# Kernel optimization log

Hardware: AMD Instinct MI355X
Metric: run time of the kernel (lower is better)

The kernel has to match this reference:

```python
import jax, jax.numpy as jnp
import numpy as np

N_NODES = 50000
N_EDGES = 1600000
N_GRAPHS = 512
HID = 64


def _mlp_params(key, din, dout, scale=0.1):
    k1, k2, k3 = jax.random.split(key, 3)
    return (
        jax.random.normal(k1, (din, HID), jnp.float32) * scale, jnp.zeros((HID,), jnp.float32),
        jax.random.normal(k2, (HID, HID), jnp.float32) * scale, jnp.zeros((HID,), jnp.float32),
        jax.random.normal(k3, (HID, dout), jnp.float32) * scale, jnp.zeros((dout,), jnp.float32),
    )


def _mlp(x, w1, b1, w2, b2, w3, b3, out_act=None):
    h = jax.nn.relu(x @ w1 + b1)
    h = jax.nn.relu(h @ w2 + b2)
    o = h @ w3 + b3
    return o if out_act is None else out_act(o)


def setup_inputs() -> dict:
    key = jax.random.key(0)
    ks = jax.random.split(key, 8)
    nf = jax.random.normal(ks[0], (N_NODES, 1), jnp.float32)
    ef = jax.random.normal(ks[1], (N_EDGES, 1), jnp.float32)
    src = jax.random.randint(ks[2], (N_EDGES,), 0, N_NODES)
    dst = jax.random.randint(ks[3], (N_EDGES,), 0, N_NODES)
    graph_id = jnp.sort(jax.random.randint(ks[4], (N_NODES,), 0, N_GRAPHS))
    e_w1, e_b1, e_w2, e_b2, e_w3, e_b3 = _mlp_params(ks[5], 3, 1)   # edge model: [src_nf, dst_nf, ef] -> msg
    n_w1, n_b1, n_w2, n_b2, n_w3, n_b3 = _mlp_params(ks[6], 2, 1)   # node model: [nf, agg] -> unf
    m_w1, m_b1, m_w2, m_b2, m_w3, m_b3 = _mlp_params(ks[7], 1, 1)   # node-wise MLP with Sigmoid out_act
    return dict(nf=nf, ef=ef, src=src, dst=dst, graph_id=graph_id,
                e_w1=e_w1, e_b1=e_b1, e_w2=e_w2, e_b2=e_b2, e_w3=e_w3, e_b3=e_b3,
                n_w1=n_w1, n_b1=n_b1, n_w2=n_w2, n_b2=n_b2, n_w3=n_w3, n_b3=n_b3,
                m_w1=m_w1, m_b1=m_b1, m_w2=m_w2, m_b2=m_b2, m_w3=m_w3, m_b3=m_b3)


def reference(nf, ef, src, dst, graph_id,
              e_w1, e_b1, e_w2, e_b2, e_w3, e_b3,
              n_w1, n_b1, n_w2, n_b2, n_w3, n_b3,
              m_w1, m_b1, m_w2, m_b2, m_w3, m_b3):
    # MPNN layer: message on edges, sum-aggregate to dst nodes, node update
    em_in = jnp.concatenate([nf[src], nf[dst], ef], axis=-1)          # [E, 3]
    msg = _mlp(em_in, e_w1, e_b1, e_w2, e_b2, e_w3, e_b3)             # [E, 1]
    agg = jax.ops.segment_sum(msg, dst, num_segments=N_NODES)        # [N, 1]
    unf = _mlp(jnp.concatenate([nf, agg], axis=-1),
               n_w1, n_b1, n_w2, n_b2, n_w3, n_b3)                    # [N, 1]
    # node-wise MLP with Sigmoid output activation
    node_out = _mlp(unf, m_w1, m_b1, m_w2, m_b2, m_w3, m_b3,
                    out_act=jax.nn.sigmoid)                           # [N, 1]
    # sum readout per graph, then final sigmoid
    rd = jax.ops.segment_sum(node_out, graph_id, num_segments=N_GRAPHS)  # [G, 1]
    return jax.nn.sigmoid(rd)
```

## Files before the change

### kernel.cpp

```cpp
#include <hip/hip_runtime.h>
#include <math.h>

#define HID 64
#define BKT_SHIFT 13
#define BKT_RANGE 8192
#define CCHUNK 32

typedef __attribute__((ext_vector_type(8))) short short8;
typedef __attribute__((ext_vector_type(4))) float f32x4;
typedef unsigned long long ull;

union FragU {
    uint4 q;
    short8 v;
    uint32_t u[4];
};

__device__ __forceinline__ uint32_t cvt_pk_bf16(float lo, float hi) {
    uint32_t r;
    asm("v_cvt_pk_bf16_f32 %0, %1, %2" : "=v"(r) : "v"(lo), "v"(hi));
    return r;
}
__device__ __forceinline__ float bf16lo_f(uint32_t u) { return __uint_as_float(u << 16); }
__device__ __forceinline__ float bf16hi_f(uint32_t u) { return __uint_as_float(u & 0xFFFF0000u); }
__device__ __forceinline__ unsigned short bf16_of(float v) {
    return (unsigned short)(cvt_pk_bf16(v, 0.f) & 0xFFFFu);
}

__global__ void prep_kernel(
    const float* __restrict__ w1,  const float* __restrict__ b1,  const float* __restrict__ w2,
    const float* __restrict__ nw1, const float* __restrict__ nb1, const float* __restrict__ nw2,
    const float* __restrict__ mw1, const float* __restrict__ mb1, const float* __restrict__ mw2,
    unsigned short* __restrict__ w1x,  unsigned short* __restrict__ w2T,
    unsigned short* __restrict__ nw1x, unsigned short* __restrict__ nw2T,
    unsigned short* __restrict__ mw1x, unsigned short* __restrict__ mw2T)
{
    int t = blockIdx.x * 256 + threadIdx.x;
    if (t < 4096) {
        int j = t >> 6, k = t & 63;
        w2T [t] = bf16_of(w2 [k * HID + j]);
        nw2T[t] = bf16_of(nw2[k * HID + j]);
        mw2T[t] = bf16_of(mw2[k * HID + j]);
    }
    if (t < 512) {
        int j = t >> 3, k = t & 7;
        float ve = k == 0 ? w1[j] : k == 1 ? w1[HID + j] : k == 2 ? w1[2 * HID + j] : k == 3 ? b1[j] : 0.f;
        float vn = k == 0 ? nw1[j] : k == 1 ? nw1[HID + j] : k == 2 ? nb1[j] : 0.f;
        float vm = k == 0 ? mw1[j] : k == 1 ? mb1[j] : 0.f;
        w1x [t] = bf16_of(ve);
        nw1x[t] = bf16_of(vn);
        mw1x[t] = bf16_of(vm);
    }
}

__global__ __launch_bounds__(256, 4) void edge_mfma6_kernel(
    const float* __restrict__ nf, const float* __restrict__ ef,
    const int* __restrict__ src, const int* __restrict__ dst,
    const unsigned short* __restrict__ w1x, const unsigned short* __restrict__ w2T,
    const float* __restrict__ b2, const float* __restrict__ w3, const float* __restrict__ b3,
    uint2* __restrict__ recs, ull* __restrict__ offs,
    float* __restrict__ aggFb, int E, int B, int nbatch, int mode)
{
    __shared__ uint2 tile[4][2][16][16];

    const int tid  = threadIdx.x;
    const int lane = tid & 63;
    const int wid  = tid >> 6;
    const int g    = lane >> 4;
    const int eL   = lane & 15;

    FragU af1[4];
#pragma unroll
    for (int t = 0; t < 4; ++t) {
        uint4 q = *(const uint4*)&w1x[(t * 16 + eL) * 8];
        af1[t].q = (g == 0) ? q : make_uint4(0, 0, 0, 0);
    }
    FragU af2[4][2];
#pragma unroll
    for (int t = 0; t < 4; ++t)
#pragma unroll
        for (int h = 0; h < 2; ++h)
            af2[t][h].q = *(const uint4*)&w2T[(t * 16 + eL) * 64 + h * 32 + g * 8];

    f32x4 b2v4[4];
    uint32_t w3p[8];
#pragma unroll
    for (int t = 0; t < 4; ++t) {
        int j = t * 16 + g * 4;
        b2v4[t] = *(const f32x4*)&b2[j];
        f32x4 wv = *(const f32x4*)&w3[j];
        w3p[2 * t]     = cvt_pk_bf16(wv[0], wv[1]);
        w3p[2 * t + 1] = cvt_pk_bf16(wv[2], wv[3]);
    }
    const float b3c = b3[0];

    int bi   = blockIdx.x;
    if (bi >= nbatch) return;
    int eidx = bi * 256 + tid;
    int ei   = eidx < E ? eidx : E - 1;
    int dcur = dst[ei];
    float a  = nf[src[ei]];
    float b  = nf[dcur];
    float c  = ef[ei];

    for (;;) {
        const int nbi   = bi + gridDim.x;
        const bool hn   = nbi < nbatch;
        const int neidx = hn ? nbi * 256 + tid : eidx;
        const int nei   = neidx < E ? neidx : E - 1;
        const int ns    = src[nei];
        const int nd    = dst[nei];
        const float ncf = ef[nei];

        float na = 0.f, nb = 0.f;
        float mymsg = 0.f;

#pragma unroll
        for (int ph = 0; ph < 2; ++ph) {
#pragma unroll
            for (int ss = 0; ss < 2; ++ss) {
                const int s = 2 * ph + ss;
                float av = __shfl(a, s * 16 + eL);
                float bv = __shfl(b, s * 16 + eL);
                float cv = __shfl(c, s * 16 + eL);
                FragU bin;
                bin.u[0] = (g == 0) ? cvt_pk_bf16(av, bv) : 0u;
                bin.u[1] = (g == 0) ? cvt_pk_bf16(cv, 1.0f) : 0u;
                bin.u[2] = 0u; bin.u[3] = 0u;
#pragma unroll
                for (int t = 0; t < 4; ++t) {
                    f32x4 h4 = __builtin_amdgcn_mfma_f32_16x16x32_bf16(
                        af1[t].v, bin.v, (f32x4){0.f, 0.f, 0.f, 0.f}, 0, 0, 0);
                    uint32_t p0 = cvt_pk_bf16(fmaxf(h4[0], 0.f), fmaxf(h4[1], 0.f));
                    uint32_t p1 = cvt_pk_bf16(fmaxf(h4[2], 0.f), fmaxf(h4[3], 0.f));
                    tile[wid][ss][eL][(4 * t + g) ^ ((eL & 7) << 1)] = make_uint2(p0, p1);
                }
            }

            if (ph == 0) {
                na = nf[ns];
                nb = nf[nd];
            }

#pragma unroll
            for (int ss = 0; ss < 2; ++ss) {
                const int s = 2 * ph + ss;
                const uint4* row = (const uint4*)&tile[wid][ss][eL][0];
                FragU bf0, bf1;
                bf0.q = row[(g)     ^ (eL & 7)];
                bf1.q = row[(4 + g) ^ (eL & 7)];

                float q0, q1, q2, q3;
                {
                    f32x4 ac = __builtin_amdgcn_mfma_f32_16x16x32_bf16(af2[0][0].v, bf0.v, b2v4[0], 0, 0, 0);
                    ac = __builtin_amdgcn_mfma_f32_16x16x32_bf16(af2[0][1].v, bf1.v, ac, 0, 0, 0);
                    q0 = fmaxf(ac[0], 0.f) * bf16lo_f(w3p[0]);
                    q0 = fmaf(fmaxf(ac[1], 0.f), bf16hi_f(w3p[0]), q0);
                    q0 = fmaf(fmaxf(ac[2], 0.f), bf16lo_f(w3p[1]), q0);
                    q0 = fmaf(fmaxf(ac[3], 0.f), bf16hi_f(w3p[1]), q0);
                }
                {
                    f32x4 ac = __builtin_amdgcn_mfma_f32_16x16x32_bf16(af2[1][0].v, bf0.v, b2v4[1], 0, 0, 0);
                    ac = __builtin_amdgcn_mfma_f32_16x16x32_bf16(af2[1][1].v, bf1.v, ac, 0, 0, 0);
                    q1 = fmaxf(ac[0], 0.f) * bf16lo_f(w3p[2]);
                    q1 = fmaf(fmaxf(ac[1], 0.f), bf16hi_f(w3p[2]), q1);
                    q1 = fmaf(fmaxf(ac[2], 0.f), bf16lo_f(w3p[3]), q1);
                    q1 = fmaf(fmaxf(ac[3], 0.f), bf16hi_f(w3p[3]), q1);
                }
                {
                    f32x4 ac = __builtin_amdgcn_mfma_f32_16x16x32_bf16(af2[2][0].v, bf0.v, b2v4[2], 0, 0, 0);
                    ac = __builtin_amdgcn_mfma_f32_16x16x32_bf16(af2[2][1].v, bf1.v, ac, 0, 0, 0);
                    q2 = fmaxf(ac[0], 0.f) * bf16lo_f(w3p[4]);
                    q2 = fmaf(fmaxf(ac[1], 0.f), bf16hi_f(w3p[4]), q2);
                    q2 = fmaf(fmaxf(ac[2], 0.f), bf16lo_f(w3p[5]), q2);
                    q2 = fmaf(fmaxf(ac[3], 0.f), bf16hi_f(w3p[5]), q2);
                }
                {
                    f32x4 ac = __builtin_amdgcn_mfma_f32_16x16x32_bf16(af2[3][0].v, bf0.v, b2v4[3], 0, 0, 0);
                    ac = __builtin_amdgcn_mfma_f32_16x16x32_bf16(af2[3][1].v, bf1.v, ac, 0, 0, 0);
                    q3 = fmaxf(ac[0], 0.f) * bf16lo_f(w3p[6]);
                    q3 = fmaf(fmaxf(ac[1], 0.f), bf16hi_f(w3p[6]), q3);
                    q3 = fmaf(fmaxf(ac[2], 0.f), bf16lo_f(w3p[7]), q3);
                    q3 = fmaf(fmaxf(ac[3], 0.f), bf16hi_f(w3p[7]), q3);
                }
                float p = (q0 + q1) + (q2 + q3);
                p += __shfl_xor(p, 16);
                p += __shfl_xor(p, 32);
                if (s == g) mymsg = p + b3c;
            }
        }

        const bool valid = eidx < E;

        if (mode == 1) {
            if (valid) atomicAdd(&aggFb[dcur], mymsg);
        } else {
            const int bkt = dcur >> BKT_SHIFT;
            const ull lt = (1ull << lane) - 1;
            int myslot = 0;
            int off = 0;
            uint32_t pack_lo = 0, pack_hi = 0;
            for (int bb = 0; bb < B; ++bb) {
                if (bb < 4) pack_lo |= (uint32_t)off << (8 * bb);
                else        pack_hi |= (uint32_t)off << (8 * (bb - 4));
                ull m = __ballot(valid && bkt == bb);
                if (valid && bkt == bb) myslot = off + (int)__popcll(m & lt);
                off += (int)__popcll(m);
            }
            pack_hi |= (uint32_t)off << 24;

            const size_t wgl = (size_t)bi * 4 + wid;
            if (valid) recs[wgl * 64 + myslot] = make_uint2((uint32_t)dcur, __float_as_uint(mymsg));
            if (lane == 0) offs[wgl] = ((ull)pack_hi << 32) | (ull)pack_lo;
        }

        if (!hn) break;
        bi = nbi; eidx = neidx; ei = nei;
        a = na; b = nb; c = ncf; dcur = nd;
    }
}

__global__ __launch_bounds__(256) void bucket_accum_kernel(
    const uint2* __restrict__ recs, const ull* __restrict__ offs,
    float* __restrict__ partial, int NW, int B)
{
    __shared__ float acc[BKT_RANGE];

    const int b = blockIdx.x / CCHUNK;
    const int c = blockIdx.x % CCHUNK;

    for (int i = threadIdx.x; i < BKT_RANGE; i += 256) acc[i] = 0.f;
    __syncthreads();

    const int wpc = (NW + CCHUNK - 1) / CCHUNK;
    const int w0 = c * wpc;
    const int w1 = (w0 + wpc < NW) ? w0 + wpc : NW;
    const int nb = b + 1;
    const int base_node = b << BKT_SHIFT;

    for (int w = w0 + threadIdx.x; w < w1; w += 256) {
        ull ov = offs[w];
        uint32_t lo = (uint32_t)ov, hi = (uint32_t)(ov >> 32);
        int ob = (int)(((b  < 4) ? (lo >> (8 * b))  : (hi >> (8 * (b  - 4)))) & 0xFF);
        int oe = (int)(((nb < 4) ? (lo >> (8 * nb)) : (hi >> (8 * (nb - 4)))) & 0xFF);
        const uint2* rb = recs + (size_t)w * 64;
        for (int r = ob; r < oe; ++r) {
            uint2 rec = rb[r];
            atomicAdd(&acc[(int)rec.x - base_node], __uint_as_float(rec.y));
        }
    }
    __syncthreads();

    float* pb = partial + ((size_t)b * CCHUNK + c) * BKT_RANGE;
    for (int i = threadIdx.x; i < BKT_RANGE; i += 256) pb[i] = acc[i];
}

__global__ __launch_bounds__(256) void bucket_reduce_kernel(
    const float* __restrict__ partial, float* __restrict__ agg, int N)
{
    int n = blockIdx.x * 256 + threadIdx.x;
    if (n >= N) return;
    int b = n >> BKT_SHIFT, nl = n & (BKT_RANGE - 1);
    const float* p = partial + (size_t)b * CCHUNK * BKT_RANGE + nl;
    float s = 0.f;
#pragma unroll 8
    for (int c = 0; c < CCHUNK; ++c) s += p[(size_t)c * BKT_RANGE];
    agg[n] = s;
}

__global__ __launch_bounds__(256, 2) void node_mfma3_kernel(
    const float* __restrict__ nf, const float* __restrict__ agg,
    const int* __restrict__ gid,
    const unsigned short* __restrict__ nw1x, const unsigned short* __restrict__ nw2T,
    const float* __restrict__ nb2, const float* __restrict__ nw3, const float* __restrict__ nb3,
    const unsigned short* __restrict__ mw1x, const unsigned short* __restrict__ mw2T,
    const float* __restrict__ mb2, const float* __restrict__ mw3, const float* __restrict__ mb3,
    float* __restrict__ rd, int N)
{
    __shared__ uint2 tile[4][4][16][16];

    const int tid  = threadIdx.x;
    const int lane = tid & 63;
    const int wid  = tid >> 6;
    const int g    = lane >> 4;
    const int eL   = lane & 15;

    const int idx = blockIdx.x * 256 + tid;
    const int i   = idx < N ? idx : N - 1;
    const float x0 = nf[i];
    const float x1 = agg[i];
    const int   gg = gid[i];

    float myunf = 0.f, o = 0.f;

    {
        FragU af1[4], af2[4][2];
        f32x4 b2v4[4]; uint32_t w3p[8];
#pragma unroll
        for (int t = 0; t < 4; ++t) {
            uint4 q = *(const uint4*)&nw1x[(t * 16 + eL) * 8];
            af1[t].q = (g == 0) ? q : make_uint4(0, 0, 0, 0);
#pragma unroll
            for (int h = 0; h < 2; ++h)
                af2[t][h].q = *(const uint4*)&nw2T[(t * 16 + eL) * 64 + h * 32 + g * 8];
            int j = t * 16 + g * 4;
            b2v4[t] = *(const f32x4*)&nb2[j];
            f32x4 wv = *(const f32x4*)&nw3[j];
            w3p[2 * t]     = cvt_pk_bf16(wv[0], wv[1]);
            w3p[2 * t + 1] = cvt_pk_bf16(wv[2], wv[3]);
        }

#pragma unroll
        for (int s = 0; s < 4; ++s) {
            float av = __shfl(x0, s * 16 + eL);
            float bv = __shfl(x1, s * 16 + eL);
            FragU bin;
            bin.u[0] = (g == 0) ? cvt_pk_bf16(av, bv) : 0u;
            bin.u[1] = (g == 0) ? cvt_pk_bf16(1.0f, 0.f) : 0u;
            bin.u[2] = 0u; bin.u[3] = 0u;
#pragma unroll
            for (int t = 0; t < 4; ++t) {
                f32x4 h4 = __builtin_amdgcn_mfma_f32_16x16x32_bf16(
                    af1[t].v, bin.v, (f32x4){0.f, 0.f, 0.f, 0.f}, 0, 0, 0);
                uint32_t p0 = cvt_pk_bf16(fmaxf(h4[0], 0.f), fmaxf(h4[1], 0.f));
                uint32_t p1 = cvt_pk_bf16(fmaxf(h4[2], 0.f), fmaxf(h4[3], 0.f));
                tile[wid][s][eL][(4 * t + g) ^ ((eL & 7) << 1)] = make_uint2(p0, p1);
            }
        }
#pragma unroll
        for (int s = 0; s < 4; ++s) {
            const uint4* row = (const uint4*)&tile[wid][s][eL][0];
            FragU bf0, bf1;
            bf0.q = row[(g)     ^ (eL & 7)];
            bf1.q = row[(4 + g) ^ (eL & 7)];
            float p = 0.f;
#pragma unroll
            for (int t = 0; t < 4; ++t) {
                f32x4 ac = __builtin_amdgcn_mfma_f32_16x16x32_bf16(af2[t][0].v, bf0.v, b2v4[t], 0, 0, 0);
                ac = __builtin_amdgcn_mfma_f32_16x16x32_bf16(af2[t][1].v, bf1.v, ac, 0, 0, 0);
                p = fmaf(fmaxf(ac[0], 0.f), bf16lo_f(w3p[2 * t]),     p);
                p = fmaf(fmaxf(ac[1], 0.f), bf16hi_f(w3p[2 * t]),     p);
                p = fmaf(fmaxf(ac[2], 0.f), bf16lo_f(w3p[2 * t + 1]), p);
                p = fmaf(fmaxf(ac[3], 0.f), bf16hi_f(w3p[2 * t + 1]), p);
            }
            p += __shfl_xor(p, 16);
            p += __shfl_xor(p, 32);
            if (s == g) myunf = p + nb3[0];
        }
    }

    {
        FragU af1[4], af2[4][2];
        f32x4 b2v4[4]; uint32_t w3p[8];
#pragma unroll
        for (int t = 0; t < 4; ++t) {
            uint4 q = *(const uint4*)&mw1x[(t * 16 + eL) * 8];
            af1[t].q = (g == 0) ? q : make_uint4(0, 0, 0, 0);
#pragma unroll
            for (int h = 0; h < 2; ++h)
                af2[t][h].q = *(const uint4*)&mw2T[(t * 16 + eL) * 64 + h * 32 + g * 8];
            int j = t * 16 + g * 4;
            b2v4[t] = *(const f32x4*)&mb2[j];
            f32x4 wv = *(const f32x4*)&mw3[j];
            w3p[2 * t]     = cvt_pk_bf16(wv[0], wv[1]);
            w3p[2 * t + 1] = cvt_pk_bf16(wv[2], wv[3]);
        }

#pragma unroll
        for (int s = 0; s < 4; ++s) {
            float uv = __shfl(myunf, s * 16 + eL);
            FragU bin;
            bin.u[0] = (g == 0) ? cvt_pk_bf16(uv, 1.0f) : 0u;
            bin.u[1] = 0u; bin.u[2] = 0u; bin.u[3] = 0u;
#pragma unroll
            for (int t = 0; t < 4; ++t) {
                f32x4 h4 = __builtin_amdgcn_mfma_f32_16x16x32_bf16(
                    af1[t].v, bin.v, (f32x4){0.f, 0.f, 0.f, 0.f}, 0, 0, 0);
                uint32_t p0 = cvt_pk_bf16(fmaxf(h4[0], 0.f), fmaxf(h4[1], 0.f));
                uint32_t p1 = cvt_pk_bf16(fmaxf(h4[2], 0.f), fmaxf(h4[3], 0.f));
                tile[wid][s][eL][(4 * t + g) ^ ((eL & 7) << 1)] = make_uint2(p0, p1);
            }
        }
#pragma unroll
        for (int s = 0; s < 4; ++s) {
            const uint4* row = (const uint4*)&tile[wid][s][eL][0];
            FragU bf0, bf1;
            bf0.q = row[(g)     ^ (eL & 7)];
            bf1.q = row[(4 + g) ^ (eL & 7)];
            float p = 0.f;
#pragma unroll
            for (int t = 0; t < 4; ++t) {
                f32x4 ac = __builtin_amdgcn_mfma_f32_16x16x32_bf16(af2[t][0].v, bf0.v, b2v4[t], 0, 0, 0);
                ac = __builtin_amdgcn_mfma_f32_16x16x32_bf16(af2[t][1].v, bf1.v, ac, 0, 0, 0);
                p = fmaf(fmaxf(ac[0], 0.f), bf16lo_f(w3p[2 * t]),     p);
                p = fmaf(fmaxf(ac[1], 0.f), bf16hi_f(w3p[2 * t]),     p);
                p = fmaf(fmaxf(ac[2], 0.f), bf16lo_f(w3p[2 * t + 1]), p);
                p = fmaf(fmaxf(ac[3], 0.f), bf16hi_f(w3p[2 * t + 1]), p);
            }
            p += __shfl_xor(p, 16);
            p += __shfl_xor(p, 32);
            if (s == g) o = p + mb3[0];
        }
    }

    const float node_out = 1.0f / (1.0f + expf(-o));

    {
        const bool ok = idx < N;
        float v = ok ? node_out : 0.0f;
        int ggv = gg;
#pragma unroll
        for (int d = 1; d < 64; d <<= 1) {
            float vup = __shfl_up(v, d);
            int   gup = __shfl_up(ggv, d);
            if (lane >= d && gup == ggv) v += vup;
        }
        int gdn = __shfl_down(ggv, 1);
        bool tail = (lane == 63) || (gdn != ggv);
        if (tail)
            atomicAdd(&rd[ggv], v);
    }
}

__global__ void readout_kernel(const float* __restrict__ rd,
                               float* __restrict__ out, int G)
{
    int g = blockIdx.x * blockDim.x + threadIdx.x;
    if (g < G) out[g] = 1.0f / (1.0f + expf(-rd[g]));
}

extern "C" void kernel_launch(void* const* d_in, const int* in_sizes, int n_in,
                              void* d_out, int out_size, void* d_ws, size_t ws_size,
                              hipStream_t stream)
{
    const float* nf  = (const float*)d_in[0];
    const float* ef  = (const float*)d_in[1];
    const int*   src = (const int*)  d_in[2];
    const int*   dst = (const int*)  d_in[3];
    const int*   gid = (const int*)  d_in[4];

    const float* e_w1 = (const float*)d_in[5];
    const float* e_b1 = (const float*)d_in[6];
    const float* e_w2 = (const float*)d_in[7];
    const float* e_b2 = (const float*)d_in[8];
    const float* e_w3 = (const float*)d_in[9];
    const float* e_b3 = (const float*)d_in[10];

    const float* n_w1 = (const float*)d_in[11];
    const float* n_b1 = (const float*)d_in[12];
    const float* n_w2 = (const float*)d_in[13];
    const float* n_b2 = (const float*)d_in[14];
    const float* n_w3 = (const float*)d_in[15];
    const float* n_b3 = (const float*)d_in[16];

    const float* m_w1 = (const float*)d_in[17];
    const float* m_b1 = (const float*)d_in[18];
    const float* m_w2 = (const float*)d_in[19];
    const float* m_b2 = (const float*)d_in[20];
    const float* m_w3 = (const float*)d_in[21];
    const float* m_b3 = (const float*)d_in[22];

    const int N = in_sizes[0];
    const int E = in_sizes[2];
    const int G = out_size;

    const int nbatch = (E + 255) / 256;
    const int NW = (E + 63) / 64;
    const int B  = (N + BKT_RANGE - 1) / BKT_RANGE;

    size_t wts_b  = 32 * 1024;
    size_t recs_b = (size_t)NW * 64 * sizeof(uint2);
    size_t offs_b = (size_t)NW * sizeof(ull);
    size_t part_b = (size_t)B * CCHUNK * BKT_RANGE * sizeof(float);
    size_t need   = wts_b + recs_b + offs_b + part_b + ((size_t)N + G) * sizeof(float);
    bool bucketok = (B <= 8) && (need <= ws_size);

    char* wp = (char*)d_ws;
    unsigned short* w1x  = (unsigned short*)(wp);
    unsigned short* nw1x = (unsigned short*)(wp + 1024);
    unsigned short* mw1x = (unsigned short*)(wp + 2048);
    unsigned short* w2T  = (unsigned short*)(wp + 4096);
    unsigned short* nw2T = (unsigned short*)(wp + 4096 + 8192);
    unsigned short* mw2T = (unsigned short*)(wp + 4096 + 16384);

    float* out = (float*)d_out;

    prep_kernel<<<16, 256, 0, stream>>>(
        e_w1, e_b1, e_w2, n_w1, n_b1, n_w2, m_w1, m_b1, m_w2,
        w1x, w2T, nw1x, nw2T, mw1x, mw2T);

    int egrid = nbatch < 2048 ? nbatch : 2048;

    if (bucketok) {
        uint2* recs    = (uint2*)(wp + wts_b);
        ull*   offs    = (ull*)(wp + wts_b + recs_b);
        float* partial = (float*)(wp + wts_b + recs_b + offs_b);
        float* agg     = (float*)(wp + wts_b + recs_b + offs_b + part_b);
        float* rd      = agg + N;

        hipMemsetAsync(rd, 0, (size_t)G * sizeof(float), stream);

        edge_mfma6_kernel<<<egrid, 256, 0, stream>>>(
            nf, ef, src, dst, w1x, w2T, e_b2, e_w3, e_b3,
            recs, offs, nullptr, E, B, nbatch, 0);

        bucket_accum_kernel<<<B * CCHUNK, 256, 0, stream>>>(
            recs, offs, partial, NW, B);

        bucket_reduce_kernel<<<(N + 255) / 256, 256, 0, stream>>>(
            partial, agg, N);

        node_mfma3_kernel<<<(N + 255) / 256, 256, 0, stream>>>(
            nf, agg, gid,
            nw1x, nw2T, n_b2, n_w3, n_b3,
            mw1x, mw2T, m_b2, m_w3, m_b3,
            rd, N);

        readout_kernel<<<(G + 255) / 256, 256, 0, stream>>>(rd, out, G);
    } else {
        float* agg = (float*)(wp + wts_b);
        float* rd  = agg + N;

        hipMemsetAsync(agg, 0, ((size_t)N + G) * sizeof(float), stream);

        edge_mfma6_kernel<<<egrid, 256, 0, stream>>>(
            nf, ef, src, dst, w1x, w2T, e_b2, e_w3, e_b3,
            nullptr, nullptr, agg, E, B, nbatch, 1);

        node_mfma3_kernel<<<(N + 255) / 256, 256, 0, stream>>>(
            nf, agg, gid,
            nw1x, nw2T, n_b2, n_w3, n_b3,
            mw1x, mw2T, m_b2, m_w3, m_b3,
            rd, N);

        readout_kernel<<<(G + 255) / 256, 256, 0, stream>>>(rd, out, G);
    }
}
```

Before: 79.82 us.

## Fuse bucket reduce into node kernel, fold memset, keep w3 in fp32, tune edge kernel

The separate bucket_reduce kernel is removed. The node kernel now sums the per-chunk partial planes directly, and the readout-buffer memset moves into block 0 of bucket_accum. Together these drop two launches and one write/read round trip of the agg array. The last-layer w3 weights stay in fp32 instead of being rounded to bf16, which removes the unpack ops and changes numerics slightly. The edge kernel's launch_bounds occupancy hint drops from 4 to 2, and s_setprio raises wave priority around the second-layer MFMA block. The rd zeroing in block 0 relies on the earlier kernel ordering, and node_mfma4 must finish before the readout kernel runs.

Result: no change. 78.41 us (-1.8%).

```diff
diff --git a/kernel.cpp b/kernel.cpp
--- a/kernel.cpp
+++ b/kernel.cpp
@@ -21,8 +21,6 @@
     asm("v_cvt_pk_bf16_f32 %0, %1, %2" : "=v"(r) : "v"(lo), "v"(hi));
     return r;
 }
-__device__ __forceinline__ float bf16lo_f(uint32_t u) { return __uint_as_float(u << 16); }
-__device__ __forceinline__ float bf16hi_f(uint32_t u) { return __uint_as_float(u & 0xFFFF0000u); }
 __device__ __forceinline__ unsigned short bf16_of(float v) {
     return (unsigned short)(cvt_pk_bf16(v, 0.f) & 0xFFFFu);
 }
@@ -53,7 +51,7 @@
     }
 }
 
-__global__ __launch_bounds__(256, 4) void edge_mfma6_kernel(
+__global__ __launch_bounds__(256, 2) void edge_mfma7_kernel(
     const float* __restrict__ nf, const float* __restrict__ ef,
     const int* __restrict__ src, const int* __restrict__ dst,
     const unsigned short* __restrict__ w1x, const unsigned short* __restrict__ w2T,
@@ -82,15 +80,12 @@
         for (int h = 0; h < 2; ++h)
             af2[t][h].q = *(const uint4*)&w2T[(t * 16 + eL) * 64 + h * 32 + g * 8];
 
-    f32x4 b2v4[4];
-    uint32_t w3p[8];
+    f32x4 b2v4[4], w3v4[4];
 #pragma unroll
     for (int t = 0; t < 4; ++t) {
         int j = t * 16 + g * 4;
         b2v4[t] = *(const f32x4*)&b2[j];
-        f32x4 wv = *(const f32x4*)&w3[j];
-        w3p[2 * t]     = cvt_pk_bf16(wv[0], wv[1]);
-        w3p[2 * t + 1] = cvt_pk_bf16(wv[2], wv[3]);
+        w3v4[t] = *(const f32x4*)&w3[j];
     }
     const float b3c = b3[0];
 
@@ -142,6 +137,7 @@
                 nb = nf[nd];
             }
 
+            __builtin_amdgcn_s_setprio(1);
 #pragma unroll
             for (int ss = 0; ss < 2; ++ss) {
                 const int s = 2 * ph + ss;
@@ -154,40 +150,41 @@
                 {
                     f32x4 ac = __builtin_amdgcn_mfma_f32_16x16x32_bf16(af2[0][0].v, bf0.v, b2v4[0], 0, 0, 0);
                     ac = __builtin_amdgcn_mfma_f32_16x16x32_bf16(af2[0][1].v, bf1.v, ac, 0, 0, 0);
-                    q0 = fmaxf(ac[0], 0.f) * bf16lo_f(w3p[0]);
-                    q0 = fmaf(fmaxf(ac[1], 0.f), bf16hi_f(w3p[0]), q0);
-                    q0 = fmaf(fmaxf(ac[2], 0.f), bf16lo_f(w3p[1]), q0);
-                    q0 = fmaf(fmaxf(ac[3], 0.f), bf16hi_f(w3p[1]), q0);
+                    q0 = fmaxf(ac[0], 0.f) * w3v4[0][0];
+                    q0 = fmaf(fmaxf(ac[1], 0.f), w3v4[0][1], q0);
+                    q0 = fmaf(fmaxf(ac[2], 0.f), w3v4[0][2], q0);
+                    q0 = fmaf(fmaxf(ac[3], 0.f), w3v4[0][3], q0);
                 }
                 {
                     f32x4 ac = __builtin_amdgcn_mfma_f32_16x16x32_bf16(af2[1][0].v, bf0.v, b2v4[1], 0, 0, 0);
                     ac = __builtin_amdgcn_mfma_f32_16x16x32_bf16(af2[1][1].v, bf1.v, ac, 0, 0, 0);
-                    q1 = fmaxf(ac[0], 0.f) * bf16lo_f(w3p[2]);
-                    q1 = fmaf(fmaxf(ac[1], 0.f), bf16hi_f(w3p[2]), q1);
-                    q1 = fmaf(fmaxf(ac[2], 0.f), bf16lo_f(w3p[3]), q1);
-                    q1 = fmaf(fmaxf(ac[3], 0.f), bf16hi_f(w3p[3]), q1);
+                    q1 = fmaxf(ac[0], 0.f) * w3v4[1][0];
+                    q1 = fmaf(fmaxf(ac[1], 0.f), w3v4[1][1], q1);
+                    q1 = fmaf(fmaxf(ac[2], 0.f), w3v4[1][2], q1);
+                    q1 = fmaf(fmaxf(ac[3], 0.f), w3v4[1][3], q1);
                 }
                 {
                     f32x4 ac = __builtin_amdgcn_mfma_f32_16x16x32_bf16(af2[2][0].v, bf0.v, b2v4[2], 0, 0, 0);
                     ac = __builtin_amdgcn_mfma_f32_16x16x32_bf16(af2[2][1].v, bf1.v, ac, 0, 0, 0);
-                    q2 = fmaxf(ac[0], 0.f) * bf16lo_f(w3p[4]);
-                    q2 = fmaf(fmaxf(ac[1], 0.f), bf16hi_f(w3p[4]), q2);
-                    q2 = fmaf(fmaxf(ac[2], 0.f), bf16lo_f(w3p[5]), q2);
-                    q2 = fmaf(fmaxf(ac[3], 0.f), bf16hi_f(w3p[5]), q2);
+                    q2 = fmaxf(ac[0], 0.f) * w3v4[2][0];
+                    q2 = fmaf(fmaxf(ac[1], 0.f), w3v4[2][1], q2);
+                    q2 = fmaf(fmaxf(ac[2], 0.f), w3v4[2][2], q2);
+                    q2 = fmaf(fmaxf(ac[3], 0.f), w3v4[2][3], q2);
                 }
                 {
                     f32x4 ac = __builtin_amdgcn_mfma_f32_16x16x32_bf16(af2[3][0].v, bf0.v, b2v4[3], 0, 0, 0);
                     ac = __builtin_amdgcn_mfma_f32_16x16x32_bf16(af2[3][1].v, bf1.v, ac, 0, 0, 0);
-                    q3 = fmaxf(ac[0], 0.f) * bf16lo_f(w3p[6]);
-                    q3 = fmaf(fmaxf(ac[1], 0.f), bf16hi_f(w3p[6]), q3);
-                    q3 = fmaf(fmaxf(ac[2], 0.f), bf16lo_f(w3p[7]), q3);
-                    q3 = fmaf(fmaxf(ac[3], 0.f), bf16hi_f(w3p[7]), q3);
+                    q3 = fmaxf(ac[0], 0.f) * w3v4[3][0];
+                    q3 = fmaf(fmaxf(ac[1], 0.f), w3v4[3][1], q3);
+                    q3 = fmaf(fmaxf(ac[2], 0.f), w3v4[3][2], q3);
+                    q3 = fmaf(fmaxf(ac[3], 0.f), w3v4[3][3], q3);
                 }
                 float p = (q0 + q1) + (q2 + q3);
                 p += __shfl_xor(p, 16);
                 p += __shfl_xor(p, 32);
                 if (s == g) mymsg = p + b3c;
             }
+            __builtin_amdgcn_s_setprio(0);
         }
 
         const bool valid = eidx < E;
@@ -222,12 +219,15 @@
 
 __global__ __launch_bounds__(256) void bucket_accum_kernel(
     const uint2* __restrict__ recs, const ull* __restrict__ offs,
-    float* __restrict__ partial, int NW, int B)
+    float* __restrict__ partial, float* __restrict__ rd, int G, int NW, int B)
 {
     __shared__ float acc[BKT_RANGE];
 
     const int b = blockIdx.x / CCHUNK;
     const int c = blockIdx.x % CCHUNK;
+
+    if (blockIdx.x == 0)
+        for (int i = threadIdx.x; i < G; i += 256) rd[i] = 0.f;
 
     for (int i = threadIdx.x; i < BKT_RANGE; i += 256) acc[i] = 0.f;
     __syncthreads();
@@ -255,21 +255,9 @@
     for (int i = threadIdx.x; i < BKT_RANGE; i += 256) pb[i] = acc[i];
 }
 
-__global__ __launch_bounds__(256) void bucket_reduce_kernel(
-    const float* __restrict__ partial, float* __restrict__ agg, int N)
-{
-    int n = blockIdx.x * 256 + threadIdx.x;
-    if (n >= N) return;
-    int b = n >> BKT_SHIFT, nl = n & (BKT_RANGE - 1);
-    const float* p = partial + (size_t)b * CCHUNK * BKT_RANGE + nl;
-    float s = 0.f;
-#pragma unroll 8
-    for (int c = 0; c < CCHUNK; ++c) s += p[(size_t)c * BKT_RANGE];
-    agg[n] = s;
-}
-
-__global__ __launch_bounds__(256, 2) void node_mfma3_kernel(
-    const float* __restrict__ nf, const float* __restrict__ agg,
+__global__ __launch_bounds__(256, 2) void node_mfma4_kernel(
+    const float* __restrict__ nf, const float* __restrict__ partial,
+    const float* __restrict__ aggFb, int nplanes,
     const int* __restrict__ gid,
     const unsigned short* __restrict__ nw1x, const unsigned short* __restrict__ nw2T,
     const float* __restrict__ nb2, const float* __restrict__ nw3, const float* __restrict__ nb3,
@@ -288,14 +276,24 @@
     const int idx = blockIdx.x * 256 + tid;
     const int i   = idx < N ? idx : N - 1;
     const float x0 = nf[i];
-    const float x1 = agg[i];
     const int   gg = gid[i];
+
+    float x1;
+    if (nplanes == 1) {
+        x1 = aggFb[i];
+    } else {
+        int bb = i >> BKT_SHIFT, nl = i & (BKT_RANGE - 1);
+        const float* p = partial + (size_t)bb * CCHUNK * BKT_RANGE + nl;
+        x1 = 0.f;
+#pragma unroll 8
+        for (int c = 0; c < CCHUNK; ++c) x1 += p[(size_t)c * BKT_RANGE];
+    }
 
     float myunf = 0.f, o = 0.f;
 
     {
         FragU af1[4], af2[4][2];
-        f32x4 b2v4[4]; uint32_t w3p[8];
+        f32x4 b2v4[4], w3v4[4];
 #pragma unroll
         for (int t = 0; t < 4; ++t) {
             uint4 q = *(const uint4*)&nw1x[(t * 16 + eL) * 8];
@@ -305,9 +303,7 @@
                 af2[t][h].q = *(const uint4*)&nw2T[(t * 16 + eL) * 64 + h * 32 + g * 8];
             int j = t * 16 + g * 4;
             b2v4[t] = *(const f32x4*)&nb2[j];
-            f32x4 wv = *(const f32x4*)&nw3[j];
-            w3p[2 * t]     = cvt_pk_bf16(wv[0], wv[1]);
-            w3p[2 * t + 1] = cvt_pk_bf16(wv[2], wv[3]);
+            w3v4[t] = *(const f32x4*)&nw3[j];
         }
 
 #pragma unroll
@@ -338,10 +334,10 @@
             for (int t = 0; t < 4; ++t) {
                 f32x4 ac = __builtin_amdgcn_mfma_f32_16x16x32_bf16(af2[t][0].v, bf0.v, b2v4[t], 0, 0, 0);
                 ac = __builtin_amdgcn_mfma_f32_16x16x32_bf16(af2[t][1].v, bf1.v, ac, 0, 0, 0);
-                p = fmaf(fmaxf(ac[0], 0.f), bf16lo_f(w3p[2 * t]),     p);
-                p = fmaf(fmaxf(ac[1], 0.f), bf16hi_f(w3p[2 * t]),     p);
-                p = fmaf(fmaxf(ac[2], 0.f), bf16lo_f(w3p[2 * t + 1]), p);
-                p = fmaf(fmaxf(ac[3], 0.f), bf16hi_f(w3p[2 * t + 1]), p);
+                p = fmaf(fmaxf(ac[0], 0.f), w3v4[t][0], p);
+                p = fmaf(fmaxf(ac[1], 0.f), w3v4[t][1], p);
+                p = fmaf(fmaxf(ac[2], 0.f), w3v4[t][2], p);
+                p = fmaf(fmaxf(ac[3], 0.f), w3v4[t][3], p);
             }
             p += __shfl_xor(p, 16);
             p += __shfl_xor(p, 32);
@@ -351,7 +347,7 @@
 
     {
         FragU af1[4], af2[4][2];
-        f32x4 b2v4[4]; uint32_t w3p[8];
+        f32x4 b2v4[4], w3v4[4];
 #pragma unroll
         for (int t = 0; t < 4; ++t) {
             uint4 q = *(const uint4*)&mw1x[(t * 16 + eL) * 8];
@@ -361,9 +357,7 @@
                 af2[t][h].q = *(const uint4*)&mw2T[(t * 16 + eL) * 64 + h * 32 + g * 8];
             int j = t * 16 + g * 4;
             b2v4[t] = *(const f32x4*)&mb2[j];
-            f32x4 wv = *(const f32x4*)&mw3[j];
-            w3p[2 * t]     = cvt_pk_bf16(wv[0], wv[1]);
-            w3p[2 * t + 1] = cvt_pk_bf16(wv[2], wv[3]);
+            w3v4[t] = *(const f32x4*)&mw3[j];
         }
 
 #pragma unroll
@@ -392,10 +386,10 @@
             for (int t = 0; t < 4; ++t) {
                 f32x4 ac = __builtin_amdgcn_mfma_f32_16x16x32_bf16(af2[t][0].v, bf0.v, b2v4[t], 0, 0, 0);
                 ac = __builtin_amdgcn_mfma_f32_16x16x32_bf16(af2[t][1].v, bf1.v, ac, 0, 0, 0);
-                p = fmaf(fmaxf(ac[0], 0.f), bf16lo_f(w3p[2 * t]),     p);
-                p = fmaf(fmaxf(ac[1], 0.f), bf16hi_f(w3p[2 * t]),     p);
-                p = fmaf(fmaxf(ac[2], 0.f), bf16lo_f(w3p[2 * t + 1]), p);
-                p = fmaf(fmaxf(ac[3], 0.f), bf16hi_f(w3p[2 * t + 1]), p);
+                p = fmaf(fmaxf(ac[0], 0.f), w3v4[t][0], p);
+                p = fmaf(fmaxf(ac[1], 0.f), w3v4[t][1], p);
+                p = fmaf(fmaxf(ac[2], 0.f), w3v4[t][2], p);
+                p = fmaf(fmaxf(ac[3], 0.f), w3v4[t][3], p);
             }
             p += __shfl_xor(p, 16);
             p += __shfl_xor(p, 32);
@@ -472,7 +466,7 @@
     size_t recs_b = (size_t)NW * 64 * sizeof(uint2);
     size_t offs_b = (size_t)NW * sizeof(ull);
     size_t part_b = (size_t)B * CCHUNK * BKT_RANGE * sizeof(float);
-    size_t need   = wts_b + recs_b + offs_b + part_b + ((size_t)N + G) * sizeof(float);
+    size_t need   = wts_b + recs_b + offs_b + part_b + (size_t)G * sizeof(float);
     bool bucketok = (B <= 8) && (need <= ws_size);
 
     char* wp = (char*)d_ws;
@@ -495,23 +489,17 @@
         uint2* recs    = (uint2*)(wp + wts_b);
         ull*   offs    = (ull*)(wp + wts_b + recs_b);
         float* partial = (float*)(wp + wts_b + recs_b + offs_b);
-        float* agg     = (float*)(wp + wts_b + recs_b + offs_b + part_b);
-        float* rd      = agg + N;
-
-        hipMemsetAsync(rd, 0, (size_t)G * sizeof(float), stream);
-
-        edge_mfma6_kernel<<<egrid, 256, 0, stream>>>(
+        float* rd      = (float*)(wp + wts_b + recs_b + offs_b + part_b);
+
+        edge_mfma7_kernel<<<egrid, 256, 0, stream>>>(
             nf, ef, src, dst, w1x, w2T, e_b2, e_w3, e_b3,
             recs, offs, nullptr, E, B, nbatch, 0);
 
         bucket_accum_kernel<<<B * CCHUNK, 256, 0, stream>>>(
-            recs, offs, partial, NW, B);
-
-        bucket_reduce_kernel<<<(N + 255) / 256, 256, 0, stream>>>(
-            partial, agg, N);
-
-        node_mfma3_kernel<<<(N + 255) / 256, 256, 0, stream>>>(
-            nf, agg, gid,
+            recs, offs, partial, rd, G, NW, B);
+
+        node_mfma4_kernel<<<(N + 255) / 256, 256, 0, stream>>>(
+            nf, partial, nullptr, CCHUNK, gid,
             nw1x, nw2T, n_b2, n_w3, n_b3,
             mw1x, mw2T, m_b2, m_w3, m_b3,
             rd, N);
@@ -523,12 +511,12 @@
 
         hipMemsetAsync(agg, 0, ((size_t)N + G) * sizeof(float), stream);
 
-        edge_mfma6_kernel<<<egrid, 256, 0, stream>>>(
+        edge_mfma7_kernel<<<egrid, 256, 0, stream>>>(
             nf, ef, src, dst, w1x, w2T, e_b2, e_w3, e_b3,
             nullptr, nullptr, agg, E, B, nbatch, 1);
 
-        node_mfma3_kernel<<<(N + 255) / 256, 256, 0, stream>>>(
-            nf, agg, gid,
+        node_mfma4_kernel<<<(N + 255) / 256, 256, 0, stream>>>(
+            nf, nullptr, agg, 1, gid,
             nw1x, nw2T, n_b2, n_w3, n_b3,
             mw1x, mw2T, m_b2, m_w3, m_b3,
             rd, N);
```
